# Performance work log

Measured on AMD Instinct MI355X. Metric: run time of the kernel, lower is better.

The kernel has to match this reference:

```python
import jax, jax.numpy as jnp
import numpy as np

N_HEADS = 16

def _rotate_half(x):
    half = x.shape[-1] // 2
    x1, x2 = x[..., :half], x[..., half:]
    return jnp.concatenate([-x2, x1], axis=-1)

def setup_inputs() -> dict:
    key = jax.random.key(0)
    ks = jax.random.split(key, 6)
    B, L, D = 8, 1024, 1280
    hd = D // N_HEADS
    return {
        "hidden_states": jax.random.normal(ks[0], (B, L, D), dtype=jnp.float32),
        "rotary_pos_emb": jax.random.normal(ks[1], (L, hd // 2), dtype=jnp.float32),
        "W_qkv": jax.random.normal(ks[2], (D, 3 * D), dtype=jnp.float32) * 0.02,
        "b_qkv": jax.random.normal(ks[3], (3 * D,), dtype=jnp.float32) * 0.02,
        "W_proj": jax.random.normal(ks[4], (D, D), dtype=jnp.float32) * 0.02,
        "b_proj": jax.random.normal(ks[5], (D,), dtype=jnp.float32) * 0.02,
    }

def reference(hidden_states, rotary_pos_emb, W_qkv, b_qkv, W_proj, b_proj):
    B, L, D = hidden_states.shape
    H = N_HEADS
    hd = D // H
    # QKV projection -> [3, B, H, L, hd]
    qkv = (hidden_states @ W_qkv + b_qkv).reshape(B, L, 3, H, hd)
    qkv = jnp.transpose(qkv, (2, 0, 3, 1, 4))
    q, k, v = qkv[0], qkv[1], qkv[2]
    # rotary embedding: emb = cat([freqs, freqs]) -> [L, hd], broadcast [1,1,L,hd]
    emb = jnp.concatenate([rotary_pos_emb, rotary_pos_emb], axis=-1)
    cos = jnp.cos(emb)[None, None]
    sin = jnp.sin(emb)[None, None]
    q = q * cos + _rotate_half(q) * sin
    k = k * cos + _rotate_half(k) * sin
    # causal SDPA (cu_seqlens is None => is_causal=True)
    scale = 1.0 / jnp.sqrt(jnp.asarray(hd, dtype=q.dtype))
    scores = jnp.einsum("bhqd,bhkd->bhqk", q, k) * scale
    causal = jnp.tril(jnp.ones((L, L), dtype=bool))
    scores = jnp.where(causal, scores, jnp.finfo(scores.dtype).min)
    attn = jax.nn.softmax(scores, axis=-1)
    out = jnp.einsum("bhqk,bhkd->bhqd", attn, v)  # [B,H,L,hd]
    out = jnp.transpose(out, (0, 2, 1, 3)).reshape(B, L, D)
    return out @ W_proj + b_proj
```

## Files before the change

kernel.cpp:

```cpp
#include <hip/hip_runtime.h>
#include <hip/hip_bf16.h>
#include <stdint.h>

#define DEV static __device__ __forceinline__

typedef __attribute__((ext_vector_type(4))) float  f32x4;
typedef __attribute__((ext_vector_type(8))) __bf16 bf16x8;
typedef __attribute__((ext_vector_type(8))) unsigned short u16x8;
typedef __attribute__((ext_vector_type(4))) unsigned short u16x4;
typedef __attribute__((ext_vector_type(4))) float  fvec4;

#define SC2F 0.16129870963914802f

DEV unsigned short f2b(float f) {
  __bf16 h = (__bf16)f;
  unsigned short u; __builtin_memcpy(&u, &h, 2);
  return u;
}
DEV float b2f(unsigned short b) {
  union { unsigned int u; float f; } v; v.u = ((unsigned int)b) << 16;
  return v.f;
}
DEV bf16x8 bzero8() {
  u16x8 z = 0; bf16x8 r; __builtin_memcpy(&r, &z, 16); return r;
}

DEV void gload_lds16(const void* g, void* l) {
  __builtin_amdgcn_global_load_lds(
      (__attribute__((address_space(1))) void*)(uintptr_t)g,
      (__attribute__((address_space(3))) void*)(uintptr_t)l, 16, 0, 0);
}


__global__ void convert_bf16x4(const float* __restrict__ in,
                               unsigned short* __restrict__ out, int n4) {
  int i = blockIdx.x * 256 + threadIdx.x;
  if (i >= n4) return;
  fvec4 v = *(const fvec4*)&in[(size_t)i * 4];
  u16x4 o;
  o[0] = f2b(v[0]); o[1] = f2b(v[1]); o[2] = f2b(v[2]); o[3] = f2b(v[3]);
  *(u16x4*)&out[(size_t)i * 4] = o;
}

__global__ void transpose_f2b(const float* __restrict__ in,
                              unsigned short* __restrict__ out, int R, int C) {
  __shared__ float t[32][33];
  int c0 = blockIdx.x * 32, r0 = blockIdx.y * 32;
  int tx = threadIdx.x & 31, ty = threadIdx.x >> 5;
#pragma unroll
  for (int i = 0; i < 32; i += 8)
    t[ty + i][tx] = in[(size_t)(r0 + ty + i) * C + c0 + tx];
  __syncthreads();
#pragma unroll
  for (int i = 0; i < 32; i += 8)
    out[(size_t)(c0 + ty + i) * R + r0 + tx] = f2b(t[tx][ty + i]);
}

__global__ void rope_table(const float* __restrict__ r, float* __restrict__ c,
                           float* __restrict__ s, int n) {
  int i = blockIdx.x * 256 + threadIdx.x;
  if (i < n) { float v = r[i]; c[i] = cosf(v); s[i] = sinf(v); }
}

template <int EPI>
__global__ __launch_bounds__(256) void gemm128(
    const unsigned short* __restrict__ A, const unsigned short* __restrict__ Bt,
    const float* __restrict__ bias,
    unsigned short* __restrict__ qo, unsigned short* __restrict__ ko,
    unsigned short* __restrict__ vo, float* __restrict__ outf,
    int M, int N, int K) {
  __shared__ __align__(16) unsigned short As[128 * 64];
  __shared__ __align__(16) unsigned short Bs[128 * 64];
  const int tid = threadIdx.x;
  const int lane = tid & 63, wave = tid >> 6;
  const int wr = wave >> 1, wc = wave & 1;
  const int g = lane >> 4, lr = lane & 15;
  const int m0 = blockIdx.y * 128, n0 = blockIdx.x * 128;

  f32x4 acc[4][4];
#pragma unroll
  for (int i = 0; i < 4; ++i)
#pragma unroll
    for (int j = 0; j < 4; ++j) acc[i][j] = f32x4{0.f, 0.f, 0.f, 0.f};

  for (int k0 = 0; k0 < K; k0 += 64) {
#pragma unroll
    for (int it = 0; it < 4; ++it) {
      int e = (it * 256 + tid) * 8;
      int r = e >> 6, p = (e >> 3) & 7;
      int sc = ((p ^ (r & 7)) << 3);
      gload_lds16(&A[(size_t)(m0 + r) * K + k0 + sc], &As[e]);
      gload_lds16(&Bt[(size_t)(n0 + r) * K + k0 + sc], &Bs[e]);
    }
    __syncthreads();
#pragma unroll
    for (int kk = 0; kk < 2; ++kk) {
      bf16x8 av[4], bv[4];
#pragma unroll
      for (int mf = 0; mf < 4; ++mf) {
        int row = wr * 64 + mf * 16 + lr;
        int ch = (kk * 4 + g) ^ (row & 7);
        av[mf] = *(const bf16x8*)&As[row * 64 + ch * 8];
      }
#pragma unroll
      for (int nf = 0; nf < 4; ++nf) {
        int row = wc * 64 + nf * 16 + lr;
        int ch = (kk * 4 + g) ^ (row & 7);
        bv[nf] = *(const bf16x8*)&Bs[row * 64 + ch * 8];
      }
#pragma unroll
      for (int mf = 0; mf < 4; ++mf)
#pragma unroll
        for (int nf = 0; nf < 4; ++nf)
          acc[mf][nf] = __builtin_amdgcn_mfma_f32_16x16x32_bf16(
              av[mf], bv[nf], acc[mf][nf], 0, 0, 0);
    }
    __syncthreads();
  }

  if (EPI == 0) {
#pragma unroll
    for (int nf = 0; nf < 4; ++nf) {
      int col = n0 + wc * 64 + nf * 16 + lr;
      float bvv = bias[col];
      int s = col / 1280;
      int rem = col - s * 1280;
      int h = rem / 80, d = rem - h * 80;
      unsigned short* dst = (s == 0) ? qo : ((s == 1) ? ko : vo);
#pragma unroll
      for (int mf = 0; mf < 4; ++mf) {
#pragma unroll
        for (int r = 0; r < 4; ++r) {
          int row = m0 + wr * 64 + mf * 16 + g * 4 + r;
          int b = row >> 10, l = row & 1023;
          dst[((size_t)(b * 16 + h) * 1024 + l) * 80 + d] =
              f2b(acc[mf][nf][r] + bvv);
        }
      }
    }
  } else {
#pragma unroll
    for (int mf = 0; mf < 4; ++mf) {
#pragma unroll
      for (int r = 0; r < 4; ++r) {
        int row = m0 + wr * 64 + mf * 16 + g * 4 + r;
#pragma unroll
        for (int nf = 0; nf < 4; ++nf) {
          int col = n0 + wc * 64 + nf * 16 + lr;
          outf[(size_t)row * N + col] = acc[mf][nf][r] + bias[col];
        }
      }
    }
  }
}

__global__ void rope_apply(unsigned short* __restrict__ q0,
                           unsigned short* __restrict__ q1,
                           const float* __restrict__ cosT,
                           const float* __restrict__ sinT) {
  int i = blockIdx.x * 256 + threadIdx.x;
  if (i >= 2 * 131072 * 5) return;
  bool isq = (i < 131072 * 5);
  unsigned short* arr = isq ? q0 : q1;
  float sc = isq ? SC2F : 1.0f;
  int rem = isq ? i : (i - 131072 * 5);
  int row = rem / 5, c = rem - (rem / 5) * 5;
  int l = row & 1023;
  size_t base = (size_t)row * 80 + c * 8;
  u16x8 x1 = *(const u16x8*)&arr[base];
  u16x8 x2 = *(const u16x8*)&arr[base + 40];
  const float* cp = &cosT[l * 40 + c * 8];
  const float* sp = &sinT[l * 40 + c * 8];
  u16x8 y1, y2;
#pragma unroll
  for (int j = 0; j < 8; ++j) {
    float a = b2f(x1[j]), b = b2f(x2[j]);
    float cc = cp[j], ss = sp[j];
    y1[j] = f2b((a * cc - b * ss) * sc);
    y2[j] = f2b((b * cc + a * ss) * sc);
  }
  *(u16x8*)&arr[base] = y1;
  *(u16x8*)&arr[base + 40] = y2;
}

__global__ __launch_bounds__(256, 3) void attn_fwd(
    const unsigned short* __restrict__ q, const unsigned short* __restrict__ k,
    const unsigned short* __restrict__ v, unsigned short* __restrict__ o) {
  __shared__ __align__(16) unsigned short Ks[64 * 80];
  __shared__ __align__(16) unsigned short Vt[80 * 72];
  __shared__ __align__(16) unsigned short Ps[4][32 * 88];

  const int tid = threadIdx.x, lane = tid & 63, wave = tid >> 6;
  const int g = lane >> 4, lr = lane & 15;
  const int bid = blockIdx.x;
  const int qi = 7 - (bid >> 7);
  const int bh = bid & 127;
  const int b = bh >> 4, h = bh & 15;
  const size_t headBase = (size_t)bh * 1024 * 80;
  const int qbase = qi * 128;
  const int wmin = qbase + wave * 32;

  bf16x8 qf[2][2], qf2[2];
#pragma unroll
  for (int mf = 0; mf < 2; ++mf) {
    const unsigned short* qr = q + headBase + (size_t)(wmin + mf * 16 + lr) * 80;
    qf[mf][0] = *(const bf16x8*)(qr + g * 8);
    qf[mf][1] = *(const bf16x8*)(qr + 32 + g * 8);
    bf16x8 t = *(const bf16x8*)(qr + 64 + (g & 1) * 8);
    if (g >= 2) t = bzero8();
    qf2[mf] = t;
  }

  float m_r[2][4], l_r[2][4];
  f32x4 o_acc[2][5];
#pragma unroll
  for (int mf = 0; mf < 2; ++mf) {
#pragma unroll
    for (int r = 0; r < 4; ++r) { m_r[mf][r] = -INFINITY; l_r[mf][r] = 0.f; }
#pragma unroll
    for (int of = 0; of < 5; ++of) o_acc[mf][of] = f32x4{0.f, 0.f, 0.f, 0.f};
  }

  const int nkv = 2 * qi + 2;
  for (int kv = 0; kv < nkv; ++kv) {
    const int kvbase = kv * 64;
    __syncthreads();
    for (int idx = tid; idx < 640; idx += 256)
      gload_lds16(&k[headBase + (size_t)kvbase * 80 + idx * 8], &Ks[idx * 8]);
    for (int i = tid; i < 640; i += 256) {
      int l = i & 63, c = i >> 6;
      u16x8 val = *(const u16x8*)&v[headBase + (size_t)(kvbase + l) * 80 + c * 8];
#pragma unroll
      for (int j = 0; j < 8; ++j) Vt[(c * 8 + j) * 72 + l] = val[j];
    }
    __syncthreads();
    if (kvbase > wmin + 31) continue;
    const bool maskT = (kvbase + 63 > wmin);

    f32x4 s[2][4];
#pragma unroll
    for (int mf = 0; mf < 2; ++mf)
#pragma unroll
      for (int nf = 0; nf < 4; ++nf) s[mf][nf] = f32x4{0.f, 0.f, 0.f, 0.f};
#pragma unroll
    for (int kp = 0; kp < 2; ++kp) {
#pragma unroll
      for (int nf = 0; nf < 4; ++nf) {
        bf16x8 kb = *(const bf16x8*)&Ks[(nf * 16 + lr) * 80 + kp * 32 + g * 8];
#pragma unroll
        for (int mf = 0; mf < 2; ++mf)
          s[mf][nf] = __builtin_amdgcn_mfma_f32_16x16x32_bf16(qf[mf][kp], kb,
                                                              s[mf][nf], 0, 0, 0);
      }
    }
#pragma unroll
    for (int nf = 0; nf < 4; ++nf) {
      bf16x8 kb = *(const bf16x8*)&Ks[(nf * 16 + lr) * 80 + 64 + (g & 1) * 8];
#pragma unroll
      for (int mf = 0; mf < 2; ++mf)
        s[mf][nf] = __builtin_amdgcn_mfma_f32_16x16x32_bf16(qf2[mf], kb,
                                                            s[mf][nf], 0, 0, 0);
    }

    if (maskT) {
#pragma unroll
      for (int mf = 0; mf < 2; ++mf)
#pragma unroll
        for (int nf = 0; nf < 4; ++nf)
#pragma unroll
          for (int r = 0; r < 4; ++r)
            if (kvbase + nf * 16 + lr > wmin + mf * 16 + g * 4 + r)
              s[mf][nf][r] = -INFINITY;
    }
    float mt[2][4];
#pragma unroll
    for (int mf = 0; mf < 2; ++mf)
#pragma unroll
      for (int r = 0; r < 4; ++r)
        mt[mf][r] = fmaxf(fmaxf(s[mf][0][r], s[mf][1][r]),
                          fmaxf(s[mf][2][r], s[mf][3][r]));
#pragma unroll
    for (int d = 1; d <= 8; d <<= 1)
#pragma unroll
      for (int mf = 0; mf < 2; ++mf)
#pragma unroll
        for (int r = 0; r < 4; ++r)
          mt[mf][r] = fmaxf(mt[mf][r], __shfl_xor(mt[mf][r], d, 64));

    int ok = 1;
#pragma unroll
    for (int mf = 0; mf < 2; ++mf)
#pragma unroll
      for (int r = 0; r < 4; ++r) ok &= (mt[mf][r] <= m_r[mf][r] + 10.0f);
    const bool need = !__all(ok);
    float fr[2][4];
    if (need) {
#pragma unroll
      for (int mf = 0; mf < 2; ++mf)
#pragma unroll
        for (int r = 0; r < 4; ++r) {
          float mn = fmaxf(m_r[mf][r], mt[mf][r]);
          fr[mf][r] = exp2f(m_r[mf][r] - mn);
          m_r[mf][r] = mn;
        }
    }
    float lt[2][4] = {{0.f, 0.f, 0.f, 0.f}, {0.f, 0.f, 0.f, 0.f}};
#pragma unroll
    for (int mf = 0; mf < 2; ++mf)
#pragma unroll
      for (int nf = 0; nf < 4; ++nf)
#pragma unroll
        for (int r = 0; r < 4; ++r) {
          float p = exp2f(s[mf][nf][r] - m_r[mf][r]);
          s[mf][nf][r] = p;
          lt[mf][r] += p;
        }
#pragma unroll
    for (int d = 1; d <= 8; d <<= 1)
#pragma unroll
      for (int mf = 0; mf < 2; ++mf)
#pragma unroll
        for (int r = 0; r < 4; ++r) lt[mf][r] += __shfl_xor(lt[mf][r], d, 64);
    if (need) {
#pragma unroll
      for (int mf = 0; mf < 2; ++mf)
#pragma unroll
        for (int r = 0; r < 4; ++r) l_r[mf][r] = l_r[mf][r] * fr[mf][r] + lt[mf][r];
#pragma unroll
      for (int mf = 0; mf < 2; ++mf)
#pragma unroll
        for (int of = 0; of < 5; ++of)
#pragma unroll
          for (int r = 0; r < 4; ++r) o_acc[mf][of][r] *= fr[mf][r];
    } else {
#pragma unroll
      for (int mf = 0; mf < 2; ++mf)
#pragma unroll
        for (int r = 0; r < 4; ++r) l_r[mf][r] += lt[mf][r];
    }

#pragma unroll
    for (int mf = 0; mf < 2; ++mf)
#pragma unroll
      for (int nf = 0; nf < 4; ++nf)
#pragma unroll
        for (int r = 0; r < 4; ++r)
          Ps[wave][(mf * 16 + g * 4 + r) * 88 + nf * 16 + lr] = f2b(s[mf][nf][r]);

#pragma unroll
    for (int kk = 0; kk < 2; ++kk) {
      bf16x8 pa[2];
#pragma unroll
      for (int mf = 0; mf < 2; ++mf)
        pa[mf] = *(const bf16x8*)&Ps[wave][(mf * 16 + lr) * 88 + kk * 32 + g * 8];
#pragma unroll
      for (int of = 0; of < 5; ++of) {
        bf16x8 vv = *(const bf16x8*)&Vt[(of * 16 + lr) * 72 + kk * 32 + g * 8];
#pragma unroll
        for (int mf = 0; mf < 2; ++mf)
          o_acc[mf][of] = __builtin_amdgcn_mfma_f32_16x16x32_bf16(pa[mf], vv,
                                                                  o_acc[mf][of], 0, 0, 0);
      }
    }
  }

#pragma unroll
  for (int mf = 0; mf < 2; ++mf) {
    float inv[4];
#pragma unroll
    for (int r = 0; r < 4; ++r) inv[r] = 1.0f / l_r[mf][r];
#pragma unroll
    for (int of = 0; of < 5; ++of)
#pragma unroll
      for (int r = 0; r < 4; ++r) {
        int row = wmin + mf * 16 + g * 4 + r;
        o[((size_t)b * 1024 + row) * 1280 + h * 80 + of * 16 + lr] =
            f2b(o_acc[mf][of][r] * inv[r]);
      }
  }
}

extern "C" void kernel_launch(void* const* d_in, const int* in_sizes, int n_in,
                              void* d_out, int out_size, void* d_ws, size_t ws_size,
                              hipStream_t stream) {
  const float* X     = (const float*)d_in[0];
  const float* rp    = (const float*)d_in[1];
  const float* Wqkv  = (const float*)d_in[2];
  const float* bqkv  = (const float*)d_in[3];
  const float* Wproj = (const float*)d_in[4];
  const float* bproj = (const float*)d_in[5];
  float* out = (float*)d_out;

  char* ws = (char*)d_ws;
  unsigned short* Xb     = (unsigned short*)(ws);
  unsigned short* Wqkvt  = (unsigned short*)(ws + 20971520);
  unsigned short* Wprojt = (unsigned short*)(ws + 30801920);
  float*          cosT   = (float*)(ws + 34078720);
  float*          sinT   = (float*)(ws + 34242560);
  unsigned short* vb     = (unsigned short*)(ws + 34406400);
  unsigned short* qb     = (unsigned short*)d_out;
  unsigned short* kb     = qb + 10485760;
  unsigned short* Ob     = Xb;

  convert_bf16x4<<<10240, 256, 0, stream>>>(X, Xb, 2621440);
  transpose_f2b<<<dim3(120, 40), 256, 0, stream>>>(Wqkv, Wqkvt, 1280, 3840);
  transpose_f2b<<<dim3(40, 40), 256, 0, stream>>>(Wproj, Wprojt, 1280, 1280);
  rope_table<<<160, 256, 0, stream>>>(rp, cosT, sinT, 40960);
  gemm128<0><<<dim3(30, 64), 256, 0, stream>>>(Xb, Wqkvt, bqkv, qb, kb, vb,
                                               nullptr, 8192, 3840, 1280);
  rope_apply<<<5120, 256, 0, stream>>>(qb, kb, cosT, sinT);
  attn_fwd<<<1024, 256, 0, stream>>>(qb, kb, vb, Ob);
  gemm128<1><<<dim3(10, 64), 256, 0, stream>>>(Ob, Wprojt, bproj, nullptr,
                                               nullptr, nullptr, out, 8192, 1280, 1280);
}
```

Baseline: 412.0 us.

## Double-buffer attention K/V, widen blocks to 512 threads, swizzle GEMM grid

The attention kernel now runs 8 waves per block over 256 query rows and double-buffers the K and V tiles in LDS, prefetching the next tile while computing the current one, with a single barrier per iteration. The QK MFMA operands are swapped so each lane owns one query row, which removes most cross-lane reductions for the row max and sum and lets P be written to LDS as packed 32-bit words. The order of query tiles is permuted for load balance. The GEMMs use a 1D grid with an XCD-aware block swizzle meant to improve L2 locality. The costs are more LDS per block, shuffles to broadcast rescale factors, and coarser causal work per block.

Result: faster. 373.3 us (-9.4%).

```diff
diff --git a/kernel.cpp b/kernel.cpp
--- a/kernel.cpp
+++ b/kernel.cpp
@@ -75,7 +75,11 @@
   const int lane = tid & 63, wave = tid >> 6;
   const int wr = wave >> 1, wc = wave & 1;
   const int g = lane >> 4, lr = lane & 15;
-  const int m0 = blockIdx.y * 128, n0 = blockIdx.x * 128;
+  const int nwg = gridDim.x, cpx = nwg >> 3;
+  const int swz = (blockIdx.x & 7) * cpx + (blockIdx.x >> 3);
+  const int gx = N >> 7;
+  const int bx = swz % gx, by = swz / gx;
+  const int m0 = by * 128, n0 = bx * 128;
 
   f32x4 acc[4][4];
 #pragma unroll
@@ -183,22 +187,25 @@
   *(u16x8*)&arr[base + 40] = y2;
 }
 
-__global__ __launch_bounds__(256, 3) void attn_fwd(
+__global__ __launch_bounds__(512, 4) void attn_fwd(
     const unsigned short* __restrict__ q, const unsigned short* __restrict__ k,
     const unsigned short* __restrict__ v, unsigned short* __restrict__ o) {
-  __shared__ __align__(16) unsigned short Ks[64 * 80];
-  __shared__ __align__(16) unsigned short Vt[80 * 72];
-  __shared__ __align__(16) unsigned short Ps[4][32 * 88];
+  __shared__ __align__(16) unsigned short Ks[2][5120];
+  __shared__ __align__(16) unsigned short Vt[2][5760];
+  __shared__ __align__(16) unsigned short Ps[8][2304];
 
   const int tid = threadIdx.x, lane = tid & 63, wave = tid >> 6;
   const int g = lane >> 4, lr = lane & 15;
   const int bid = blockIdx.x;
-  const int qi = 7 - (bid >> 7);
+  const int t4 = bid >> 7;
+  const int qi = (t4 == 0) ? 3 : (t4 == 1) ? 2 : (t4 == 2) ? 0 : 1;
   const int bh = bid & 127;
   const int b = bh >> 4, h = bh & 15;
   const size_t headBase = (size_t)bh * 1024 * 80;
-  const int qbase = qi * 128;
+  const int qbase = qi * 256;
   const int wmin = qbase + wave * 32;
+  const int nkv = qi * 4 + 4;
+  const int vl = tid & 63, vc = tid >> 6;
 
   bf16x8 qf[2][2], qf2[2];
 #pragma unroll
@@ -211,172 +218,196 @@
     qf2[mf] = t;
   }
 
-  float m_r[2][4], l_r[2][4];
+  float m_r[2] = {-INFINITY, -INFINITY}, l_r[2] = {0.f, 0.f};
   f32x4 o_acc[2][5];
 #pragma unroll
+  for (int mf = 0; mf < 2; ++mf)
+#pragma unroll
+    for (int of = 0; of < 5; ++of) o_acc[mf][of] = f32x4{0.f, 0.f, 0.f, 0.f};
+
+  unsigned short* PsW = Ps[wave];
+
+  {
+    const unsigned short* vsrc = v + headBase;
+    u16x8 p0 = *(const u16x8*)&vsrc[(size_t)vl * 80 + vc * 8];
+    u16x8 p1;
+    if (tid < 128) p1 = *(const u16x8*)&vsrc[(size_t)vl * 80 + (8 + vc) * 8];
+    for (int i = tid; i < 640; i += 512)
+      gload_lds16(k + headBase + i * 8, &Ks[0][i * 8]);
+#pragma unroll
+    for (int j = 0; j < 8; ++j) Vt[0][(vc * 8 + j) * 72 + vl] = p0[j];
+    if (tid < 128) {
+#pragma unroll
+      for (int j = 0; j < 8; ++j) Vt[0][((8 + vc) * 8 + j) * 72 + vl] = p1[j];
+    }
+  }
+  __syncthreads();
+
+  for (int kv = 0; kv < nkv; ++kv) {
+    const int bufI = kv & 1, nb = bufI ^ 1;
+    const int kvbase = kv * 64;
+    const bool doStage = (kv + 1 < nkv);
+    const bool active = (kvbase <= wmin + 31);
+
+    u16x8 p0, p1;
+    if (doStage) {
+      const unsigned short* vsrc = v + headBase + (size_t)(kv + 1) * 5120;
+      p0 = *(const u16x8*)&vsrc[(size_t)vl * 80 + vc * 8];
+      if (tid < 128) p1 = *(const u16x8*)&vsrc[(size_t)vl * 80 + (8 + vc) * 8];
+      const unsigned short* ksrc = k + headBase + (size_t)(kv + 1) * 5120;
+      for (int i = tid; i < 640; i += 512)
+        gload_lds16(ksrc + i * 8, &Ks[nb][i * 8]);
+    }
+
+    if (active) {
+      const unsigned short* KsB = Ks[bufI];
+      f32x4 s[2][4];
+#pragma unroll
+      for (int mf = 0; mf < 2; ++mf)
+#pragma unroll
+        for (int nf = 0; nf < 4; ++nf) s[mf][nf] = f32x4{0.f, 0.f, 0.f, 0.f};
+#pragma unroll
+      for (int kp = 0; kp < 2; ++kp)
+#pragma unroll
+        for (int nf = 0; nf < 4; ++nf) {
+          bf16x8 kb = *(const bf16x8*)&KsB[(nf * 16 + lr) * 80 + kp * 32 + g * 8];
+#pragma unroll
+          for (int mf = 0; mf < 2; ++mf)
+            s[mf][nf] = __builtin_amdgcn_mfma_f32_16x16x32_bf16(kb, qf[mf][kp],
+                                                                s[mf][nf], 0, 0, 0);
+        }
+#pragma unroll
+      for (int nf = 0; nf < 4; ++nf) {
+        bf16x8 kb = *(const bf16x8*)&KsB[(nf * 16 + lr) * 80 + 64 + (g & 1) * 8];
+#pragma unroll
+        for (int mf = 0; mf < 2; ++mf)
+          s[mf][nf] = __builtin_amdgcn_mfma_f32_16x16x32_bf16(kb, qf2[mf],
+                                                              s[mf][nf], 0, 0, 0);
+      }
+
+      const bool maskT = (kvbase + 63 > wmin);
+      if (maskT) {
+        const int kb0 = kvbase + g * 4;
+        const int qq = wmin + lr;
+#pragma unroll
+        for (int mf = 0; mf < 2; ++mf)
+#pragma unroll
+          for (int nf = 0; nf < 4; ++nf)
+#pragma unroll
+            for (int r = 0; r < 4; ++r)
+              if (kb0 + nf * 16 + r > qq + mf * 16) s[mf][nf][r] = -INFINITY;
+      }
+      float mt[2];
+#pragma unroll
+      for (int mf = 0; mf < 2; ++mf) {
+        float a = fmaxf(fmaxf(s[mf][0][0], s[mf][0][1]), fmaxf(s[mf][0][2], s[mf][0][3]));
+        float b2 = fmaxf(fmaxf(s[mf][1][0], s[mf][1][1]), fmaxf(s[mf][1][2], s[mf][1][3]));
+        float c = fmaxf(fmaxf(s[mf][2][0], s[mf][2][1]), fmaxf(s[mf][2][2], s[mf][2][3]));
+        float d = fmaxf(fmaxf(s[mf][3][0], s[mf][3][1]), fmaxf(s[mf][3][2], s[mf][3][3]));
+        float m = fmaxf(fmaxf(a, b2), fmaxf(c, d));
+        m = fmaxf(m, __shfl_xor(m, 16, 64));
+        m = fmaxf(m, __shfl_xor(m, 32, 64));
+        mt[mf] = m;
+      }
+      int ok = (mt[0] <= m_r[0] + 10.0f) && (mt[1] <= m_r[1] + 10.0f);
+      const bool need = !__all(ok);
+      float fr[2];
+      if (need) {
+#pragma unroll
+        for (int mf = 0; mf < 2; ++mf) {
+          float mn = fmaxf(m_r[mf], mt[mf]);
+          fr[mf] = exp2f(m_r[mf] - mn);
+          m_r[mf] = mn;
+        }
+      }
+      float lt[2] = {0.f, 0.f};
+#pragma unroll
+      for (int mf = 0; mf < 2; ++mf)
+#pragma unroll
+        for (int nf = 0; nf < 4; ++nf)
+#pragma unroll
+          for (int r = 0; r < 4; ++r) {
+            float p = exp2f(s[mf][nf][r] - m_r[mf]);
+            s[mf][nf][r] = p;
+            lt[mf] += p;
+          }
+#pragma unroll
+      for (int mf = 0; mf < 2; ++mf) {
+        lt[mf] += __shfl_xor(lt[mf], 16, 64);
+        lt[mf] += __shfl_xor(lt[mf], 32, 64);
+      }
+      if (need) {
+#pragma unroll
+        for (int mf = 0; mf < 2; ++mf) {
+          l_r[mf] = l_r[mf] * fr[mf] + lt[mf];
+#pragma unroll
+          for (int r = 0; r < 4; ++r) {
+            float fro = __shfl(fr[mf], g * 4 + r, 64);
+#pragma unroll
+            for (int of = 0; of < 5; ++of) o_acc[mf][of][r] *= fro;
+          }
+        }
+      } else {
+        l_r[0] += lt[0];
+        l_r[1] += lt[1];
+      }
+
+#pragma unroll
+      for (int mf = 0; mf < 2; ++mf)
+#pragma unroll
+        for (int nf = 0; nf < 4; ++nf) {
+          unsigned w0 = (unsigned)f2b(s[mf][nf][0]) |
+                        ((unsigned)f2b(s[mf][nf][1]) << 16);
+          unsigned w1 = (unsigned)f2b(s[mf][nf][2]) |
+                        ((unsigned)f2b(s[mf][nf][3]) << 16);
+          unsigned* dst = (unsigned*)&PsW[(mf * 16 + lr) * 72 + nf * 16 + g * 4];
+          dst[0] = w0;
+          dst[1] = w1;
+        }
+    }
+
+    if (doStage) {
+#pragma unroll
+      for (int j = 0; j < 8; ++j) Vt[nb][(vc * 8 + j) * 72 + vl] = p0[j];
+      if (tid < 128) {
+#pragma unroll
+        for (int j = 0; j < 8; ++j) Vt[nb][((8 + vc) * 8 + j) * 72 + vl] = p1[j];
+      }
+    }
+
+    if (active) {
+      const unsigned short* VtB = Vt[bufI];
+#pragma unroll
+      for (int kk = 0; kk < 2; ++kk) {
+        bf16x8 pa[2];
+#pragma unroll
+        for (int mf = 0; mf < 2; ++mf)
+          pa[mf] = *(const bf16x8*)&PsW[(mf * 16 + lr) * 72 + kk * 32 + g * 8];
+#pragma unroll
+        for (int of = 0; of < 5; ++of) {
+          bf16x8 vv = *(const bf16x8*)&VtB[(of * 16 + lr) * 72 + kk * 32 + g * 8];
+#pragma unroll
+          for (int mf = 0; mf < 2; ++mf)
+            o_acc[mf][of] = __builtin_amdgcn_mfma_f32_16x16x32_bf16(
+                pa[mf], vv, o_acc[mf][of], 0, 0, 0);
+        }
+      }
+    }
+    __syncthreads();
+  }
+
+#pragma unroll
   for (int mf = 0; mf < 2; ++mf) {
-#pragma unroll
-    for (int r = 0; r < 4; ++r) { m_r[mf][r] = -INFINITY; l_r[mf][r] = 0.f; }
-#pragma unroll
-    for (int of = 0; of < 5; ++of) o_acc[mf][of] = f32x4{0.f, 0.f, 0.f, 0.f};
-  }
-
-  const int nkv = 2 * qi + 2;
-  for (int kv = 0; kv < nkv; ++kv) {
-    const int kvbase = kv * 64;
-    __syncthreads();
-    for (int idx = tid; idx < 640; idx += 256)
-      gload_lds16(&k[headBase + (size_t)kvbase * 80 + idx * 8], &Ks[idx * 8]);
-    for (int i = tid; i < 640; i += 256) {
-      int l = i & 63, c = i >> 6;
-      u16x8 val = *(const u16x8*)&v[headBase + (size_t)(kvbase + l) * 80 + c * 8];
-#pragma unroll
-      for (int j = 0; j < 8; ++j) Vt[(c * 8 + j) * 72 + l] = val[j];
-    }
-    __syncthreads();
-    if (kvbase > wmin + 31) continue;
-    const bool maskT = (kvbase + 63 > wmin);
-
-    f32x4 s[2][4];
-#pragma unroll
-    for (int mf = 0; mf < 2; ++mf)
-#pragma unroll
-      for (int nf = 0; nf < 4; ++nf) s[mf][nf] = f32x4{0.f, 0.f, 0.f, 0.f};
-#pragma unroll
-    for (int kp = 0; kp < 2; ++kp) {
-#pragma unroll
-      for (int nf = 0; nf < 4; ++nf) {
-        bf16x8 kb = *(const bf16x8*)&Ks[(nf * 16 + lr) * 80 + kp * 32 + g * 8];
-#pragma unroll
-        for (int mf = 0; mf < 2; ++mf)
-          s[mf][nf] = __builtin_amdgcn_mfma_f32_16x16x32_bf16(qf[mf][kp], kb,
-                                                              s[mf][nf], 0, 0, 0);
-      }
-    }
-#pragma unroll
-    for (int nf = 0; nf < 4; ++nf) {
-      bf16x8 kb = *(const bf16x8*)&Ks[(nf * 16 + lr) * 80 + 64 + (g & 1) * 8];
-#pragma unroll
-      for (int mf = 0; mf < 2; ++mf)
-        s[mf][nf] = __builtin_amdgcn_mfma_f32_16x16x32_bf16(qf2[mf], kb,
-                                                            s[mf][nf], 0, 0, 0);
-    }
-
-    if (maskT) {
-#pragma unroll
-      for (int mf = 0; mf < 2; ++mf)
-#pragma unroll
-        for (int nf = 0; nf < 4; ++nf)
-#pragma unroll
-          for (int r = 0; r < 4; ++r)
-            if (kvbase + nf * 16 + lr > wmin + mf * 16 + g * 4 + r)
-              s[mf][nf][r] = -INFINITY;
-    }
-    float mt[2][4];
-#pragma unroll
-    for (int mf = 0; mf < 2; ++mf)
-#pragma unroll
-      for (int r = 0; r < 4; ++r)
-        mt[mf][r] = fmaxf(fmaxf(s[mf][0][r], s[mf][1][r]),
-                          fmaxf(s[mf][2][r], s[mf][3][r]));
-#pragma unroll
-    for (int d = 1; d <= 8; d <<= 1)
-#pragma unroll
-      for (int mf = 0; mf < 2; ++mf)
-#pragma unroll
-        for (int r = 0; r < 4; ++r)
-          mt[mf][r] = fmaxf(mt[mf][r], __shfl_xor(mt[mf][r], d, 64));
-
-    int ok = 1;
-#pragma unroll
-    for (int mf = 0; mf < 2; ++mf)
-#pragma unroll
-      for (int r = 0; r < 4; ++r) ok &= (mt[mf][r] <= m_r[mf][r] + 10.0f);
-    const bool need = !__all(ok);
-    float fr[2][4];
-    if (need) {
-#pragma unroll
-      for (int mf = 0; mf < 2; ++mf)
-#pragma unroll
-        for (int r = 0; r < 4; ++r) {
-          float mn = fmaxf(m_r[mf][r], mt[mf][r]);
-          fr[mf][r] = exp2f(m_r[mf][r] - mn);
-          m_r[mf][r] = mn;
-        }
-    }
-    float lt[2][4] = {{0.f, 0.f, 0.f, 0.f}, {0.f, 0.f, 0.f, 0.f}};
-#pragma unroll
-    for (int mf = 0; mf < 2; ++mf)
-#pragma unroll
-      for (int nf = 0; nf < 4; ++nf)
-#pragma unroll
-        for (int r = 0; r < 4; ++r) {
-          float p = exp2f(s[mf][nf][r] - m_r[mf][r]);
-          s[mf][nf][r] = p;
-          lt[mf][r] += p;
-        }
-#pragma unroll
-    for (int d = 1; d <= 8; d <<= 1)
-#pragma unroll
-      for (int mf = 0; mf < 2; ++mf)
-#pragma unroll
-        for (int r = 0; r < 4; ++r) lt[mf][r] += __shfl_xor(lt[mf][r], d, 64);
-    if (need) {
-#pragma unroll
-      for (int mf = 0; mf < 2; ++mf)
-#pragma unroll
-        for (int r = 0; r < 4; ++r) l_r[mf][r] = l_r[mf][r] * fr[mf][r] + lt[mf][r];
-#pragma unroll
-      for (int mf = 0; mf < 2; ++mf)
-#pragma unroll
-        for (int of = 0; of < 5; ++of)
-#pragma unroll
-          for (int r = 0; r < 4; ++r) o_acc[mf][of][r] *= fr[mf][r];
-    } else {
-#pragma unroll
-      for (int mf = 0; mf < 2; ++mf)
-#pragma unroll
-        for (int r = 0; r < 4; ++r) l_r[mf][r] += lt[mf][r];
-    }
-
-#pragma unroll
-    for (int mf = 0; mf < 2; ++mf)
-#pragma unroll
-      for (int nf = 0; nf < 4; ++nf)
-#pragma unroll
-        for (int r = 0; r < 4; ++r)
-          Ps[wave][(mf * 16 + g * 4 + r) * 88 + nf * 16 + lr] = f2b(s[mf][nf][r]);
-
-#pragma unroll
-    for (int kk = 0; kk < 2; ++kk) {
-      bf16x8 pa[2];
-#pragma unroll
-      for (int mf = 0; mf < 2; ++mf)
-        pa[mf] = *(const bf16x8*)&Ps[wave][(mf * 16 + lr) * 88 + kk * 32 + g * 8];
-#pragma unroll
-      for (int of = 0; of < 5; ++of) {
-        bf16x8 vv = *(const bf16x8*)&Vt[(of * 16 + lr) * 72 + kk * 32 + g * 8];
-#pragma unroll
-        for (int mf = 0; mf < 2; ++mf)
-          o_acc[mf][of] = __builtin_amdgcn_mfma_f32_16x16x32_bf16(pa[mf], vv,
-                                                                  o_acc[mf][of], 0, 0, 0);
-      }
-    }
-  }
-
-#pragma unroll
-  for (int mf = 0; mf < 2; ++mf) {
-    float inv[4];
-#pragma unroll
-    for (int r = 0; r < 4; ++r) inv[r] = 1.0f / l_r[mf][r];
-#pragma unroll
-    for (int of = 0; of < 5; ++of)
-#pragma unroll
-      for (int r = 0; r < 4; ++r) {
-        int row = wmin + mf * 16 + g * 4 + r;
+    float linv = 1.0f / l_r[mf];
+#pragma unroll
+    for (int r = 0; r < 4; ++r) {
+      float li = __shfl(linv, g * 4 + r, 64);
+      int row = wmin + mf * 16 + g * 4 + r;
+#pragma unroll
+      for (int of = 0; of < 5; ++of)
         o[((size_t)b * 1024 + row) * 1280 + h * 80 + of * 16 + lr] =
-            f2b(o_acc[mf][of][r] * inv[r]);
-      }
+            f2b(o_acc[mf][of][r] * li);
+    }
   }
 }
 
@@ -406,10 +437,10 @@
   transpose_f2b<<<dim3(120, 40), 256, 0, stream>>>(Wqkv, Wqkvt, 1280, 3840);
   transpose_f2b<<<dim3(40, 40), 256, 0, stream>>>(Wproj, Wprojt, 1280, 1280);
   rope_table<<<160, 256, 0, stream>>>(rp, cosT, sinT, 40960);
-  gemm128<0><<<dim3(30, 64), 256, 0, stream>>>(Xb, Wqkvt, bqkv, qb, kb, vb,
-                                               nullptr, 8192, 3840, 1280);
+  gemm128<0><<<1920, 256, 0, stream>>>(Xb, Wqkvt, bqkv, qb, kb, vb,
+                                       nullptr, 8192, 3840, 1280);
   rope_apply<<<5120, 256, 0, stream>>>(qb, kb, cosT, sinT);
-  attn_fwd<<<1024, 256, 0, stream>>>(qb, kb, vb, Ob);
-  gemm128<1><<<dim3(10, 64), 256, 0, stream>>>(Ob, Wprojt, bproj, nullptr,
-                                               nullptr, nullptr, out, 8192, 1280, 1280);
-}
+  attn_fwd<<<512, 512, 0, stream>>>(qb, kb, vb, Ob);
+  gemm128<1><<<640, 256, 0, stream>>>(Ob, Wprojt, bproj, nullptr,
+                                      nullptr, nullptr, out, 8192, 1280, 1280);
+}
```
